# Optimization experiments

Hardware: AMD Instinct MI355X
Metric: run time of the kernel (lower is better)

## Reference

```python
import jax, jax.numpy as jnp
import numpy as np

N_USER = 200000
N_ITEM = 100000
E = 1000000
H = 128
IN_USER = 64
IN_ITEM = 128
OUT = 16
L = 2  # n_layers
NEG_SLOPE = 0.01  # F.leaky_relu default


def _leaky(x):
    return jnp.where(x >= 0, x, NEG_SLOPE * x)


def _sage(x_src, x_dst, src, dst, n_dst, Wl, bl, Wr):
    """PyG SAGEConv (aggr='mean'): lin_l(mean_{j->i} x_j) + lin_r(x_i)."""
    agg = jax.ops.segment_sum(x_src[src], dst, num_segments=n_dst)  # [n_dst, H]
    cnt = jax.ops.segment_sum(jnp.ones((src.shape[0],), x_src.dtype), dst, num_segments=n_dst)
    mean = agg / jnp.maximum(cnt, 1.0)[:, None]
    return mean @ Wl + bl + x_dst @ Wr


def setup_inputs() -> dict:
    key = jax.random.key(0)
    ks = jax.random.split(key, 32)
    s = 0.05
    inp = {
        "x_user": jax.random.normal(ks[0], (N_USER, IN_USER), jnp.float32),
        "x_item": jax.random.normal(ks[1], (N_ITEM, IN_ITEM), jnp.float32),
        "src_rates": jax.random.randint(ks[2], (E,), 0, N_USER, jnp.int32),
        "dst_rates": jax.random.randint(ks[3], (E,), 0, N_ITEM, jnp.int32),
        "src_rated": jax.random.randint(ks[4], (E,), 0, N_ITEM, jnp.int32),
        "dst_rated": jax.random.randint(ks[5], (E,), 0, N_USER, jnp.int32),
        "src_fol": jax.random.randint(ks[6], (E,), 0, N_USER, jnp.int32),
        "dst_fol": jax.random.randint(ks[7], (E,), 0, N_USER, jnp.int32),
        # input projections (per node type)
        "W_in_user": s * jax.random.normal(ks[8], (IN_USER, H), jnp.float32),
        "b_in_user": jnp.zeros((H,), jnp.float32),
        "W_in_item": s * jax.random.normal(ks[9], (IN_ITEM, H), jnp.float32),
        "b_in_item": jnp.zeros((H,), jnp.float32),
        # per-layer SAGEConv params, stacked over layers [L, ...]
        "Wl_rates": s * jax.random.normal(ks[10], (L, H, H), jnp.float32),
        "bl_rates": jnp.zeros((L, H), jnp.float32),
        "Wr_rates": s * jax.random.normal(ks[11], (L, H, H), jnp.float32),
        "Wl_rated": s * jax.random.normal(ks[12], (L, H, H), jnp.float32),
        "bl_rated": jnp.zeros((L, H), jnp.float32),
        "Wr_rated": s * jax.random.normal(ks[13], (L, H, H), jnp.float32),
        "Wl_fol": s * jax.random.normal(ks[14], (L, H, H), jnp.float32),
        "bl_fol": jnp.zeros((L, H), jnp.float32),
        "Wr_fol": s * jax.random.normal(ks[15], (L, H, H), jnp.float32),
        # output head
        "W_out": s * jax.random.normal(ks[16], (H, OUT), jnp.float32),
        "b_out": jnp.zeros((OUT,), jnp.float32),
    }
    return inp


def reference(x_user, x_item, src_rates, dst_rates, src_rated, dst_rated,
              src_fol, dst_fol, W_in_user, b_in_user, W_in_item, b_in_item,
              Wl_rates, bl_rates, Wr_rates, Wl_rated, bl_rated, Wr_rated,
              Wl_fol, bl_fol, Wr_fol, W_out, b_out):
    hu = x_user @ W_in_user + b_in_user  # [N_USER, H]
    hi = x_item @ W_in_item + b_in_item  # [N_ITEM, H]
    for l in range(L):
        # user->item ('rates')
        hi_new = _sage(hu, hi, src_rates, dst_rates, N_ITEM,
                       Wl_rates[l], bl_rates[l], Wr_rates[l])
        # item->user ('rated_by') + user->user ('follows'), HeteroConv aggr='sum'
        hu_new = (_sage(hi, hu, src_rated, dst_rated, N_USER,
                        Wl_rated[l], bl_rated[l], Wr_rated[l])
                  + _sage(hu, hu, src_fol, dst_fol, N_USER,
                          Wl_fol[l], bl_fol[l], Wr_fol[l]))
        hu, hi = hu_new, hi_new
        if l != L - 1:
            hu = _leaky(hu)
            hi = _leaky(hi)
    return hu @ W_out + b_out  # target_node == 'user'
```

## Files before the change

kernel.cpp:

```cpp
#include <hip/hip_runtime.h>
#include <cstdint>

typedef short short8 __attribute__((ext_vector_type(8)));
typedef float floatx4 __attribute__((ext_vector_type(4)));
typedef unsigned char uchar;

constexpr int NU = 200000;
constexpr int NI = 100000;
constexpr int NEDGE = 1000000;
constexpr int HD = 128;
constexpr int HH = HD * HD;
constexpr int BUK = 1024;
constexpr int EPB = 4096;
constexpr int EPT = 16;
constexpr int MAXBUK = 256;
constexpr int NBLK = (NEDGE + EPB - 1) / EPB;
constexpr int NB_I = (NI + BUK - 1) / BUK;
constexpr int NB_U = (NU + BUK - 1) / BUK;
constexpr int LROW = 136;

__device__ __forceinline__ float bits2f(short s) {
    return __uint_as_float(((unsigned int)(unsigned short)s) << 16);
}
__device__ __forceinline__ short f2bits(float f) {
    unsigned int u = __float_as_uint(f);
    unsigned int lsb = (u >> 16) & 1u;
    u += 0x7fffu + lsb;
    return (short)(u >> 16);
}

__global__ __launch_bounds__(256) void k_cnt3(const int* __restrict__ dst0,
                                              const int* __restrict__ dst1,
                                              const int* __restrict__ dst2,
                                              int* __restrict__ cnts) {
    __shared__ int cnt[MAXBUK];
    const int g = blockIdx.x / NBLK;
    const int blk = blockIdx.x % NBLK;
    const int* dst = (g == 0) ? dst0 : (g == 1) ? dst1 : dst2;
    int t = threadIdx.x;
    for (int b = t; b < MAXBUK; b += 256) cnt[b] = 0;
    __syncthreads();
    const int e0 = blk * EPB + t * EPT;
#pragma unroll
    for (int i = 0; i < EPT; ++i) {
        int e = e0 + i;
        if (e < NEDGE) atomicAdd(&cnt[dst[e] >> 10], 1);
    }
    __syncthreads();
    for (int b = t; b < MAXBUK; b += 256)
        cnts[(size_t)(g * NBLK + blk) * MAXBUK + b] = cnt[b];
}

__global__ __launch_bounds__(256) void k_bases3(const int* __restrict__ cnts,
                                                int* __restrict__ base,
                                                int* __restrict__ bbase,
                                                int* __restrict__ off0,
                                                int* __restrict__ off1,
                                                int* __restrict__ off2) {
    __shared__ int s[256];
    const int g = blockIdx.x;
    const int t = threadIdx.x;
    int tot = 0;
    for (int blk = 0; blk < NBLK; ++blk)
        tot += cnts[(size_t)(g * NBLK + blk) * MAXBUK + t];
    s[t] = tot;
    __syncthreads();
    for (int d = 1; d < 256; d <<= 1) {
        int u = (t >= d) ? s[t - d] : 0;
        __syncthreads();
        s[t] += u;
        __syncthreads();
    }
    int bb = s[t] - tot;
    bbase[g * 257 + t] = bb;
    if (t == 255) bbase[g * 257 + 256] = bb + tot;
    int run = bb;
    for (int blk = 0; blk < NBLK; ++blk) {
        size_t idx = (size_t)(g * NBLK + blk) * MAXBUK + t;
        base[idx] = run;
        run += cnts[idx];
    }
    if (t == 0) {
        if (g == 0) off0[NI] = NEDGE;
        else if (g == 1) off1[NU] = NEDGE;
        else off2[NU] = NEDGE;
    }
}

__global__ __launch_bounds__(256) void k_part3(const int* __restrict__ src0,
                                               const int* __restrict__ dst0,
                                               const int* __restrict__ src1,
                                               const int* __restrict__ dst1,
                                               const int* __restrict__ src2,
                                               const int* __restrict__ dst2,
                                               const int* __restrict__ base,
                                               int* __restrict__ pairs) {
    __shared__ int cnt[MAXBUK];
    __shared__ int bas[MAXBUK];
    const int g = blockIdx.x / NBLK;
    const int blk = blockIdx.x % NBLK;
    const int* src = (g == 0) ? src0 : (g == 1) ? src1 : src2;
    const int* dst = (g == 0) ? dst0 : (g == 1) ? dst1 : dst2;
    int* pg = pairs + (size_t)g * NEDGE;
    int t = threadIdx.x;
    for (int b = t; b < MAXBUK; b += 256) cnt[b] = 0;
    __syncthreads();
    const int e0 = blk * EPB + t * EPT;
    int sv[EPT], dv[EPT], rk[EPT];
#pragma unroll
    for (int i = 0; i < EPT; ++i) {
        int e = e0 + i;
        bool ok = e < NEDGE;
        dv[i] = ok ? dst[e] : 0;
        sv[i] = ok ? src[e] : 0;
    }
#pragma unroll
    for (int i = 0; i < EPT; ++i)
        rk[i] = (e0 + i < NEDGE) ? atomicAdd(&cnt[dv[i] >> 10], 1) : 0;
    __syncthreads();
    for (int b = t; b < MAXBUK; b += 256)
        bas[b] = base[(size_t)(g * NBLK + blk) * MAXBUK + b];
    __syncthreads();
#pragma unroll
    for (int i = 0; i < EPT; ++i) {
        if (e0 + i < NEDGE)
            pg[bas[dv[i] >> 10] + rk[i]] = sv[i] | ((dv[i] & 1023) << 18);
    }
}

__global__ __launch_bounds__(256) void k_place3(const int* __restrict__ pairs,
                                                const int* __restrict__ bbase,
                                                int* __restrict__ off0, int* __restrict__ esrc0,
                                                int* __restrict__ off1, int* __restrict__ esrc1,
                                                int* __restrict__ off2, int* __restrict__ esrc2) {
    __shared__ int cnt[BUK];
    __shared__ int ts[256];
    int bi = blockIdx.x;
    int g, bloc, N;
    int* off;
    int* esrc;
    if (bi < NB_I) { g = 0; bloc = bi; N = NI; off = off0; esrc = esrc0; }
    else if (bi < NB_I + NB_U) { g = 1; bloc = bi - NB_I; N = NU; off = off1; esrc = esrc1; }
    else { g = 2; bloc = bi - NB_I - NB_U; N = NU; off = off2; esrc = esrc2; }
    const int* pg = pairs + (size_t)g * NEDGE;
    const int b0 = bbase[g * 257 + bloc];
    const int b1 = bbase[g * 257 + bloc + 1];
    const int t = threadIdx.x;
    for (int i = t; i < BUK; i += 256) cnt[i] = 0;
    __syncthreads();
    for (int j = b0 + t; j < b1; j += 256) atomicAdd(&cnt[pg[j] >> 18], 1);
    __syncthreads();
    const int idx = t * 4;
    int c0 = cnt[idx], c1 = cnt[idx + 1], c2 = cnt[idx + 2], c3 = cnt[idx + 3];
    int ssum = c0 + c1 + c2 + c3;
    ts[t] = ssum;
    __syncthreads();
    for (int d = 1; d < 256; d <<= 1) {
        int u = (t >= d) ? ts[t - d] : 0;
        __syncthreads();
        ts[t] += u;
        __syncthreads();
    }
    int o = b0 + ts[t] - ssum;
    const int n0 = bloc * BUK;
    int cc[4] = {c0, c1, c2, c3};
#pragma unroll
    for (int i = 0; i < 4; ++i) {
        int n = n0 + idx + i;
        if (n < N) off[n] = o;
        cnt[idx + i] = o;
        o += cc[i];
    }
    __syncthreads();
    for (int j = b0 + t; j < b1; j += 256) {
        int p = pg[j];
        int pos = atomicAdd(&cnt[p >> 18], 1);
        esrc[pos] = p & 0x3FFFF;
    }
}

__global__ void k_pack(short* __restrict__ dst, const float* __restrict__ A,
                       const float* __restrict__ B, const float* __restrict__ B2,
                       int KA, int KBr, int NCOL) {
    int l = threadIdx.x;
    int kbt = (KA + KBr) >> 5;
    int nt = blockIdx.x / kbt;
    int kb = blockIdx.x % kbt;
    int col = nt * 16 + (l & 15);
    int k0 = kb * 32 + (l >> 4) * 8;
    short8 o;
#pragma unroll
    for (int j = 0; j < 8; ++j) {
        int k = k0 + j;
        float f;
        if (k < KA) {
            f = A[(size_t)k * NCOL + col];
        } else {
            int k2 = k - KA;
            f = B[(size_t)k2 * NCOL + col];
            if (B2) f += B2[(size_t)k2 * NCOL + col];
        }
        o[j] = f2bits(f);
    }
    *(short8*)(dst + ((size_t)blockIdx.x * 64 + l) * 8) = o;
}

__global__ void k_pack3(short* __restrict__ dst, const float* __restrict__ A,
                        const float* __restrict__ B, const float* __restrict__ C1,
                        const float* __restrict__ C2) {
    int l = threadIdx.x;
    constexpr int kbt = 12;
    int nt = blockIdx.x / kbt;
    int kb = blockIdx.x % kbt;
    int col = nt * 16 + (l & 15);
    int k0 = kb * 32 + (l >> 4) * 8;
    short8 o;
#pragma unroll
    for (int j = 0; j < 8; ++j) {
        int k = k0 + j;
        float f;
        if (k < 128) f = A[(size_t)k * 128 + col];
        else if (k < 256) f = B[(size_t)(k - 128) * 128 + col];
        else f = C1[(size_t)(k - 256) * 128 + col] + C2[(size_t)(k - 256) * 128 + col];
        o[j] = f2bits(f);
    }
    *(short8*)(dst + ((size_t)blockIdx.x * 64 + l) * 8) = o;
}

__global__ void k_foldW(float* __restrict__ dst, const float* __restrict__ Wa,
                        const float* __restrict__ Wb, const float* __restrict__ Wo,
                        int colOff, int NC) {
    int k = blockIdx.x;
    int c = threadIdx.x;
    float a = 0.f;
    for (int t = 0; t < 128; ++t) {
        float w = Wa[(size_t)k * 128 + t];
        if (Wb) w += Wb[(size_t)k * 128 + t];
        a += w * Wo[t * 16 + c];
    }
    dst[(size_t)k * NC + colOff + c] = a;
}

__global__ void k_bfold(float* __restrict__ dst, const float* __restrict__ bl1,
                        const float* __restrict__ bl2, const float* __restrict__ Wo,
                        const float* __restrict__ bo) {
    int c = threadIdx.x;
    float a = 0.f;
    for (int t = 0; t < 128; ++t) a += (bl1[t] + bl2[t]) * Wo[t * 16 + c];
    dst[c] = a + bo[c];
}

__global__ void k_addbias(float* __restrict__ dst, const float* __restrict__ a,
                          const float* __restrict__ b) {
    int i = threadIdx.x;
    dst[i] = a[i] + b[i];
}

__device__ __forceinline__ void gather_mean_u8(const uchar* __restrict__ X8,
                                               const float* __restrict__ scale,
                                               const int* __restrict__ off,
                                               const int* __restrict__ esrc,
                                               int ar, int g, float macc[4][8]) {
#pragma unroll
    for (int kb = 0; kb < 4; ++kb)
#pragma unroll
        for (int i = 0; i < 8; ++i) macc[kb][i] = 0.f;
    float S = 0.f;

    const int s = off[ar], e = off[ar + 1];
    for (int j = s; j < e; ++j) {
        const int i0 = esrc[j];
        const float s0 = scale[i0];
        const uchar* p0 = X8 + (size_t)i0 * HD + g * 8;
        S += s0;
#pragma unroll
        for (int kb = 0; kb < 4; ++kb) {
            uint2 v = *(const uint2*)(p0 + kb * 32);
#pragma unroll
            for (int i = 0; i < 4; ++i) {
                macc[kb][i]     = fmaf(s0, (float)((v.x >> (8 * i)) & 0xffu), macc[kb][i]);
                macc[kb][4 + i] = fmaf(s0, (float)((v.y >> (8 * i)) & 0xffu), macc[kb][4 + i]);
            }
        }
    }
    const int d = e - s;
    const float inv = 1.f / (float)(d > 0 ? d : 1);
    const float corr = 128.f * S;
#pragma unroll
    for (int kb = 0; kb < 4; ++kb)
#pragma unroll
        for (int i = 0; i < 8; ++i) macc[kb][i] = (macc[kb][i] - corr) * inv;
}

template <int NT2>
__device__ __forceinline__ void fold_epi(const floatx4* acc8, const float* __restrict__ bias,
                                         const short* __restrict__ pFold,
                                         short* __restrict__ Y, int r0, int lane,
                                         short* my, int M) {
    const int colL = lane & 15;
    const int g = lane >> 4;
#pragma unroll
    for (int nt = 0; nt < 8; ++nt) {
        float bv = bias[nt * 16 + colL];
#pragma unroll
        for (int r = 0; r < 4; ++r) {
            float x = acc8[nt][r] + bv;
            x = (x >= 0.f) ? x : 0.01f * x;
            my[(g * 4 + r) * LROW + nt * 16 + colL] = f2bits(x);
        }
    }
    short8 af[4];
    const short* rp = my + colL * LROW + g * 8;
#pragma unroll
    for (int kb = 0; kb < 4; ++kb) af[kb] = *(const short8*)(rp + kb * 32);

    floatx4 a2[NT2];
#pragma unroll
    for (int nt2 = 0; nt2 < NT2; ++nt2) a2[nt2] = (floatx4){0.f, 0.f, 0.f, 0.f};
    const short8* wp = (const short8*)pFold + lane;
#pragma unroll
    for (int nt2 = 0; nt2 < NT2; ++nt2)
#pragma unroll
        for (int kb = 0; kb < 4; ++kb) {
            short8 b = wp[(nt2 * 4 + kb) * 64];
            a2[nt2] = __builtin_amdgcn_mfma_f32_16x16x32_bf16(af[kb], b, a2[nt2], 0, 0, 0);
        }

    const int rbase = r0 + g * 4;
#pragma unroll
    for (int nt2 = 0; nt2 < NT2; ++nt2)
#pragma unroll
        for (int r = 0; r < 4; ++r) {
            int row = rbase + r;
            if (row < M) Y[(size_t)row * (NT2 * 16) + nt2 * 16 + colL] = f2bits(a2[nt2][r]);
        }
}

__global__ __launch_bounds__(256) void k_sage_all(
        const short* __restrict__ hu, const short* __restrict__ hi,
        const uchar* __restrict__ hu8, const float* __restrict__ scU,
        const uchar* __restrict__ hi8, const float* __restrict__ scI,
        const int* __restrict__ off_rates, const int* __restrict__ esrc_rates,
        const int* __restrict__ off_rated, const int* __restrict__ esrc_rated,
        const int* __restrict__ off_fol, const int* __restrict__ esrc_fol,
        const short* __restrict__ WpI, const float* __restrict__ biasI,
        const short* __restrict__ pYI,
        const short* __restrict__ WpU, const float* __restrict__ biasU,
        const short* __restrict__ pYU,
        short* __restrict__ YI, short* __restrict__ YZ, int gU) {
    __shared__ short stage[4 * 16 * LROW];
    const int lane = threadIdx.x & 63;
    const int wv = threadIdx.x >> 6;
    short* my = stage + wv * (16 * LROW);
    const int g = lane >> 4;
    const int ksub = g * 8;

    if ((int)blockIdx.x < gU) {
        const int r0 = blockIdx.x * 64 + wv * 16;
        int ar = r0 + (lane & 15);
        if (ar >= NU) ar = NU - 1;

        short8 afrag[12];
        {
            float macc[4][8];
            gather_mean_u8(hi8, scI, off_rated, esrc_rated, ar, g, macc);
#pragma unroll
            for (int kb = 0; kb < 4; ++kb) {
                short8 f;
#pragma unroll
                for (int i = 0; i < 8; ++i) f[i] = f2bits(macc[kb][i]);
                afrag[kb] = f;
            }
            gather_mean_u8(hu8, scU, off_fol, esrc_fol, ar, g, macc);
#pragma unroll
            for (int kb = 0; kb < 4; ++kb) {
                short8 f;
#pragma unroll
                for (int i = 0; i < 8; ++i) f[i] = f2bits(macc[kb][i]);
                afrag[4 + kb] = f;
            }
        }
        {
            const short* p = hu + (size_t)ar * HD + ksub;
#pragma unroll
            for (int kb = 0; kb < 4; ++kb) afrag[8 + kb] = *(const short8*)(p + kb * 32);
        }

        floatx4 acc[8];
#pragma unroll
        for (int nt = 0; nt < 8; ++nt) acc[nt] = (floatx4){0.f, 0.f, 0.f, 0.f};
        const short8* wp = (const short8*)WpU + lane;
#pragma unroll
        for (int nt = 0; nt < 8; ++nt)
#pragma unroll
            for (int kb = 0; kb < 12; ++kb) {
                short8 b = wp[(nt * 12 + kb) * 64];
                acc[nt] = __builtin_amdgcn_mfma_f32_16x16x32_bf16(afrag[kb], b, acc[nt], 0, 0, 0);
            }

        fold_epi<2>(acc, biasU, pYU, YZ, r0, lane, my, NU);
    } else {
        const int b = blockIdx.x - gU;
        const int r0 = b * 64 + wv * 16;
        int ar = r0 + (lane & 15);
        if (ar >= NI) ar = NI - 1;

        short8 afrag[8];
        {
            float macc[4][8];
            gather_mean_u8(hu8, scU, off_rates, esrc_rates, ar, g, macc);
#pragma unroll
            for (int kb = 0; kb < 4; ++kb) {
                short8 f;
#pragma unroll
                for (int i = 0; i < 8; ++i) f[i] = f2bits(macc[kb][i]);
                afrag[kb] = f;
            }
            const short* p = hi + (size_t)ar * HD + ksub;
#pragma unroll
            for (int kb = 0; kb < 4; ++kb) afrag[4 + kb] = *(const short8*)(p + kb * 32);
        }

        floatx4 acc[8];
#pragma unroll
        for (int nt = 0; nt < 8; ++nt) acc[nt] = (floatx4){0.f, 0.f, 0.f, 0.f};
        const short8* wp = (const short8*)WpI + lane;
#pragma unroll
        for (int nt = 0; nt < 8; ++nt)
#pragma unroll
            for (int kb = 0; kb < 8; ++kb) {
                short8 b = wp[(nt * 8 + kb) * 64];
                acc[nt] = __builtin_amdgcn_mfma_f32_16x16x32_bf16(afrag[kb], b, acc[nt], 0, 0, 0);
            }

        fold_epi<1>(acc, biasI, pYI, YI, r0, lane, my, NI);
    }
}

template <int KB1>
__device__ __forceinline__ void mm_body(int bid, const float* __restrict__ A1,
                                        const short* __restrict__ Wp,
                                        const float* __restrict__ bias,
                                        short* __restrict__ C,
                                        uchar* __restrict__ U8,
                                        float* __restrict__ scale, int M,
                                        int lane, int wv) {
    const int r0 = bid * 128 + wv * 32;
    const int g = lane >> 4;
    const int ksub = g * 8;
    const int colL = lane & 15;
    short8 afrag[2][KB1];
#pragma unroll
    for (int h = 0; h < 2; ++h) {
        int ar = r0 + h * 16 + colL;
        if (ar >= M) ar = M - 1;
        const float* p = A1 + (size_t)ar * (KB1 * 32) + ksub;
#pragma unroll
        for (int kb = 0; kb < KB1; ++kb) {
            short8 f;
#pragma unroll
            for (int j = 0; j < 8; ++j) f[j] = f2bits(p[kb * 32 + j]);
            afrag[h][kb] = f;
        }
    }
    floatx4 acc[2][8];
#pragma unroll
    for (int h = 0; h < 2; ++h)
#pragma unroll
        for (int nt = 0; nt < 8; ++nt) acc[h][nt] = (floatx4){0.f, 0.f, 0.f, 0.f};
    const short8* wp = (const short8*)Wp + lane;
#pragma unroll
    for (int nt = 0; nt < 8; ++nt)
#pragma unroll
        for (int kb = 0; kb < KB1; ++kb) {
            short8 b = wp[(nt * KB1 + kb) * 64];
            acc[0][nt] = __builtin_amdgcn_mfma_f32_16x16x32_bf16(afrag[0][kb], b, acc[0][nt], 0, 0, 0);
            acc[1][nt] = __builtin_amdgcn_mfma_f32_16x16x32_bf16(afrag[1][kb], b, acc[1][nt], 0, 0, 0);
        }
#pragma unroll
    for (int h = 0; h < 2; ++h) {
#pragma unroll
        for (int r = 0; r < 4; ++r) {
            const int row = r0 + h * 16 + g * 4 + r;
            float v[8];
            float m = 0.f;
#pragma unroll
            for (int nt = 0; nt < 8; ++nt) {
                v[nt] = acc[h][nt][r] + bias[nt * 16 + colL];
                m = fmaxf(m, fabsf(v[nt]));
            }
#pragma unroll
            for (int x = 1; x < 16; x <<= 1) m = fmaxf(m, __shfl_xor(m, x, 16));
            const float invq = (m > 0.f) ? 127.f / m : 0.f;
            if (row < M) {
#pragma unroll
                for (int nt = 0; nt < 8; ++nt) {
                    C[(size_t)row * HD + nt * 16 + colL] = f2bits(v[nt]);
                    U8[(size_t)row * HD + nt * 16 + colL] =
                        (uchar)((int)rintf(v[nt] * invq) + 128);
                }
                if (colL == 0) scale[row] = m * (1.f / 127.f);
            }
        }
    }
}

__global__ __launch_bounds__(256) void k_mm2(const float* __restrict__ xu,
                                             const short* __restrict__ pWu,
                                             const float* __restrict__ bu,
                                             short* __restrict__ hu,
                                             uchar* __restrict__ hu8,
                                             float* __restrict__ scU,
                                             const float* __restrict__ xi,
                                             const short* __restrict__ pWi,
                                             const float* __restrict__ bi,
                                             short* __restrict__ hi,
                                             uchar* __restrict__ hi8,
                                             float* __restrict__ scI, int gU2) {
    const int lane = threadIdx.x & 63;
    const int wv = threadIdx.x >> 6;
    if ((int)blockIdx.x < gU2)
        mm_body<2>(blockIdx.x, xu, pWu, bu, hu, hu8, scU, NU, lane, wv);
    else
        mm_body<4>(blockIdx.x - gU2, xi, pWi, bi, hi, hi8, scI, NI, lane, wv);
}

__global__ __launch_bounds__(256) void k_out(const short* __restrict__ YZ,
                                             const short* __restrict__ YI,
                                             const int* __restrict__ off_f,
                                             const int* __restrict__ esrc_f,
                                             const int* __restrict__ off_r,
                                             const int* __restrict__ esrc_r,
                                             const float* __restrict__ bias16,
                                             float* __restrict__ out, int N) {
    int t = threadIdx.x;
    int node = blockIdx.x * 128 + (t >> 1);
    int half = t & 1;
    if (node >= N) return;
    const int c0 = half * 8;

    float a[8] = {0.f, 0.f, 0.f, 0.f, 0.f, 0.f, 0.f, 0.f};
    {
        const int s = off_f[node], e = off_f[node + 1];
        int j = s;
        for (; j + 4 <= e; j += 4) {
            short8 v0 = *(const short8*)(YZ + (size_t)esrc_f[j] * 32 + c0);
            short8 v1 = *(const short8*)(YZ + (size_t)esrc_f[j + 1] * 32 + c0);
            short8 v2 = *(const short8*)(YZ + (size_t)esrc_f[j + 2] * 32 + c0);
            short8 v3 = *(const short8*)(YZ + (size_t)esrc_f[j + 3] * 32 + c0);
#pragma unroll
            for (int i = 0; i < 8; ++i)
                a[i] += (bits2f(v0[i]) + bits2f(v1[i])) + (bits2f(v2[i]) + bits2f(v3[i]));
        }
        for (; j < e; ++j) {
            short8 v = *(const short8*)(YZ + (size_t)esrc_f[j] * 32 + c0);
#pragma unroll
            for (int i = 0; i < 8; ++i) a[i] += bits2f(v[i]);
        }
        int d = e - s;
        float inv = 1.f / (float)(d > 0 ? d : 1);
#pragma unroll
        for (int i = 0; i < 8; ++i) a[i] *= inv;
    }
    {
        float b[8] = {0.f, 0.f, 0.f, 0.f, 0.f, 0.f, 0.f, 0.f};
        const int s = off_r[node], e = off_r[node + 1];
        int j = s;
        for (; j + 4 <= e; j += 4) {
            short8 v0 = *(const short8*)(YI + (size_t)esrc_r[j] * 16 + c0);
            short8 v1 = *(const short8*)(YI + (size_t)esrc_r[j + 1] * 16 + c0);
            short8 v2 = *(const short8*)(YI + (size_t)esrc_r[j + 2] * 16 + c0);
            short8 v3 = *(const short8*)(YI + (size_t)esrc_r[j + 3] * 16 + c0);
#pragma unroll
            for (int i = 0; i < 8; ++i)
                b[i] += (bits2f(v0[i]) + bits2f(v1[i])) + (bits2f(v2[i]) + bits2f(v3[i]));
        }
        for (; j < e; ++j) {
            short8 v = *(const short8*)(YI + (size_t)esrc_r[j] * 16 + c0);
#pragma unroll
            for (int i = 0; i < 8; ++i) b[i] += bits2f(v[i]);
        }
        int d = e - s;
        float inv = 1.f / (float)(d > 0 ? d : 1);
#pragma unroll
        for (int i = 0; i < 8; ++i) a[i] += b[i] * inv;
    }
    short8 z = *(const short8*)(YZ + (size_t)node * 32 + 16 + c0);
#pragma unroll
    for (int i = 0; i < 8; ++i)
        out[(size_t)node * 16 + c0 + i] = a[i] + bits2f(z[i]) + bias16[c0 + i];
}

extern "C" void kernel_launch(void* const* d_in, const int* in_sizes, int n_in,
                              void* d_out, int out_size, void* d_ws, size_t ws_size,
                              hipStream_t stream) {
    const float* x_user    = (const float*)d_in[0];
    const float* x_item    = (const float*)d_in[1];
    const int* src_rates   = (const int*)d_in[2];
    const int* dst_rates   = (const int*)d_in[3];
    const int* src_rated   = (const int*)d_in[4];
    const int* dst_rated   = (const int*)d_in[5];
    const int* src_fol     = (const int*)d_in[6];
    const int* dst_fol     = (const int*)d_in[7];
    const float* W_in_user = (const float*)d_in[8];
    const float* b_in_user = (const float*)d_in[9];
    const float* W_in_item = (const float*)d_in[10];
    const float* b_in_item = (const float*)d_in[11];
    const float* Wl_rates  = (const float*)d_in[12];
    const float* bl_rates  = (const float*)d_in[13];
    const float* Wr_rates  = (const float*)d_in[14];
    const float* Wl_rated  = (const float*)d_in[15];
    const float* bl_rated  = (const float*)d_in[16];
    const float* Wr_rated  = (const float*)d_in[17];
    const float* Wl_fol    = (const float*)d_in[18];
    const float* bl_fol    = (const float*)d_in[19];
    const float* Wr_fol    = (const float*)d_in[20];
    const float* W_out     = (const float*)d_in[21];
    const float* b_out     = (const float*)d_in[22];
    float* out = (float*)d_out;

    char* w = (char*)d_ws;
    size_t used = 0;
    auto alloc = [&](size_t bytes) -> void* {
        void* p = w + used;
        used += (bytes + 255) & ~(size_t)255;
        return p;
    };
    short* hu_a = (short*)alloc((size_t)NU * HD * 2);
    short* hi_a = (short*)alloc((size_t)NI * HD * 2);
    uchar* hu8  = (uchar*)alloc((size_t)NU * HD);
    uchar* hi8  = (uchar*)alloc((size_t)NI * HD);
    float* scU  = (float*)alloc((size_t)NU * 4);
    float* scI  = (float*)alloc((size_t)NI * 4);
    short* YZ   = (short*)alloc((size_t)NU * 32 * 2);
    short* YI   = (short*)alloc((size_t)NI * 16 * 2);

    int* off_rates  = (int*)alloc((size_t)(NI + 1) * 4);
    int* esrc_rates = (int*)alloc((size_t)NEDGE * 4);
    int* off_rated  = (int*)alloc((size_t)(NU + 1) * 4);
    int* esrc_rated = (int*)alloc((size_t)NEDGE * 4);
    int* off_fol    = (int*)alloc((size_t)(NU + 1) * 4);
    int* esrc_fol   = (int*)alloc((size_t)NEDGE * 4);
    int* pairs      = (int*)alloc((size_t)3 * NEDGE * 4);
    int* cnts       = (int*)alloc((size_t)3 * NBLK * MAXBUK * 4);
    int* base       = (int*)alloc((size_t)3 * NBLK * MAXBUK * 4);
    int* bbase      = (int*)alloc((size_t)3 * 257 * 4);

    short* pWu     = (short*)alloc(8 * 2 * 64 * 8 * 2);
    short* pWi     = (short*)alloc(8 * 4 * 64 * 8 * 2);
    short* pRates0 = (short*)alloc(8 * 8 * 64 * 8 * 2);
    short* pUser0  = (short*)alloc(8 * 12 * 64 * 8 * 2);
    float* WfU     = (float*)alloc(128 * 32 * 4);
    float* WfI     = (float*)alloc(128 * 16 * 4);
    short* pYU     = (short*)alloc(2 * 4 * 64 * 8 * 2);
    short* pYI     = (short*)alloc(1 * 4 * 64 * 8 * 2);
    float* bSum0   = (float*)alloc(128 * 4);
    float* bias16  = (float*)alloc(16 * 4);
    if (used > ws_size) return;

    k_cnt3<<<3 * NBLK, 256, 0, stream>>>(dst_rates, dst_rated, dst_fol, cnts);
    k_bases3<<<3, 256, 0, stream>>>(cnts, base, bbase, off_rates, off_rated, off_fol);
    k_part3<<<3 * NBLK, 256, 0, stream>>>(src_rates, dst_rates, src_rated, dst_rated,
                                          src_fol, dst_fol, base, pairs);
    k_place3<<<NB_I + 2 * NB_U, 256, 0, stream>>>(pairs, bbase,
                                                  off_rates, esrc_rates,
                                                  off_rated, esrc_rated,
                                                  off_fol, esrc_fol);

    k_pack<<<16, 64, 0, stream>>>(pWu, W_in_user, nullptr, nullptr, 64, 0, 128);
    k_pack<<<32, 64, 0, stream>>>(pWi, W_in_item, nullptr, nullptr, 128, 0, 128);
    k_pack<<<64, 64, 0, stream>>>(pRates0, Wl_rates, Wr_rates, nullptr, 128, 128, 128);
    k_pack3<<<96, 64, 0, stream>>>(pUser0, Wl_rated, Wl_fol, Wr_rated, Wr_fol);
    k_addbias<<<1, 128, 0, stream>>>(bSum0, bl_rated, bl_fol);
    k_foldW<<<128, 16, 0, stream>>>(WfU, Wl_fol + HH,   nullptr,     W_out, 0, 32);
    k_foldW<<<128, 16, 0, stream>>>(WfU, Wr_rated + HH, Wr_fol + HH, W_out, 16, 32);
    k_foldW<<<128, 16, 0, stream>>>(WfI, Wl_rated + HH, nullptr,     W_out, 0, 16);
    k_pack<<<8, 64, 0, stream>>>(pYU, WfU, nullptr, nullptr, 128, 0, 32);
    k_pack<<<4, 64, 0, stream>>>(pYI, WfI, nullptr, nullptr, 128, 0, 16);
    k_bfold<<<1, 16, 0, stream>>>(bias16, bl_rated + 128, bl_fol + 128, W_out, b_out);

    const int gU2 = (NU + 127) / 128;
    const int gI2 = (NI + 127) / 128;
    const int gU  = (NU + 63) / 64;
    const int gI  = (NI + 63) / 64;

    k_mm2<<<gU2 + gI2, 256, 0, stream>>>(x_user, pWu, b_in_user, hu_a, hu8, scU,
                                         x_item, pWi, b_in_item, hi_a, hi8, scI, gU2);

    k_sage_all<<<gU + gI, 256, 0, stream>>>(
        hu_a, hi_a, hu8, scU, hi8, scI,
        off_rates, esrc_rates, off_rated, esrc_rated, off_fol, esrc_fol,
        pRates0, bl_rates, pYI, pUser0, bSum0, pYU, YI, YZ, gU);

    k_out<<<(NU + 127) / 128, 256, 0, stream>>>(
        YZ, YI, off_fol, esrc_fol, off_rated, esrc_rated, bias16, out, NU);
}
```

Before: 494.8 us.

## Permute uint8 feature layout for 32-byte contiguous gathers and unroll edge loop by four

The quantized uint8 node features are now written in a permuted column order, so each lane group's 32 bytes are contiguous. The gather can then load two uint4 per neighbor instead of four strided uint2. The edge loop is also unrolled by four so several neighbor rows are loaded before the accumulate, which is meant to raise memory-level parallelism in the gather that dominates the runtime. This relies on the producer's permutation matching the consumer's macc index mapping, and the unroll costs extra registers.

Result: faster. 448.5 us (-9.4%).

```diff
diff --git a/kernel.cpp b/kernel.cpp
--- a/kernel.cpp
+++ b/kernel.cpp
@@ -256,6 +256,20 @@
     dst[i] = a[i] + b[i];
 }
 
+__device__ __forceinline__ void acc_u8(float macc[4][8], uint4 a, uint4 b, float s) {
+#pragma unroll
+    for (int i = 0; i < 4; ++i) {
+        macc[0][i]     = fmaf(s, (float)((a.x >> (8 * i)) & 0xffu), macc[0][i]);
+        macc[0][4 + i] = fmaf(s, (float)((a.y >> (8 * i)) & 0xffu), macc[0][4 + i]);
+        macc[1][i]     = fmaf(s, (float)((a.z >> (8 * i)) & 0xffu), macc[1][i]);
+        macc[1][4 + i] = fmaf(s, (float)((a.w >> (8 * i)) & 0xffu), macc[1][4 + i]);
+        macc[2][i]     = fmaf(s, (float)((b.x >> (8 * i)) & 0xffu), macc[2][i]);
+        macc[2][4 + i] = fmaf(s, (float)((b.y >> (8 * i)) & 0xffu), macc[2][4 + i]);
+        macc[3][i]     = fmaf(s, (float)((b.z >> (8 * i)) & 0xffu), macc[3][i]);
+        macc[3][4 + i] = fmaf(s, (float)((b.w >> (8 * i)) & 0xffu), macc[3][4 + i]);
+    }
+}
+
 __device__ __forceinline__ void gather_mean_u8(const uchar* __restrict__ X8,
                                                const float* __restrict__ scale,
                                                const int* __restrict__ off,
@@ -268,20 +282,31 @@
     float S = 0.f;
 
     const int s = off[ar], e = off[ar + 1];
-    for (int j = s; j < e; ++j) {
+    int j = s;
+    for (; j + 4 <= e; j += 4) {
+        const int i0 = esrc[j], i1 = esrc[j + 1], i2 = esrc[j + 2], i3 = esrc[j + 3];
+        const float s0 = scale[i0], s1 = scale[i1], s2 = scale[i2], s3 = scale[i3];
+        const uchar* p0 = X8 + (size_t)i0 * HD + g * 32;
+        const uchar* p1 = X8 + (size_t)i1 * HD + g * 32;
+        const uchar* p2 = X8 + (size_t)i2 * HD + g * 32;
+        const uchar* p3 = X8 + (size_t)i3 * HD + g * 32;
+        uint4 a0 = *(const uint4*)p0, b0 = *(const uint4*)(p0 + 16);
+        uint4 a1 = *(const uint4*)p1, b1 = *(const uint4*)(p1 + 16);
+        uint4 a2 = *(const uint4*)p2, b2 = *(const uint4*)(p2 + 16);
+        uint4 a3 = *(const uint4*)p3, b3 = *(const uint4*)(p3 + 16);
+        S += (s0 + s1) + (s2 + s3);
+        acc_u8(macc, a0, b0, s0);
+        acc_u8(macc, a1, b1, s1);
+        acc_u8(macc, a2, b2, s2);
+        acc_u8(macc, a3, b3, s3);
+    }
+    for (; j < e; ++j) {
         const int i0 = esrc[j];
         const float s0 = scale[i0];
-        const uchar* p0 = X8 + (size_t)i0 * HD + g * 8;
+        const uchar* p0 = X8 + (size_t)i0 * HD + g * 32;
+        uint4 a = *(const uint4*)p0, b = *(const uint4*)(p0 + 16);
         S += s0;
-#pragma unroll
-        for (int kb = 0; kb < 4; ++kb) {
-            uint2 v = *(const uint2*)(p0 + kb * 32);
-#pragma unroll
-            for (int i = 0; i < 4; ++i) {
-                macc[kb][i]     = fmaf(s0, (float)((v.x >> (8 * i)) & 0xffu), macc[kb][i]);
-                macc[kb][4 + i] = fmaf(s0, (float)((v.y >> (8 * i)) & 0xffu), macc[kb][4 + i]);
-            }
-        }
+        acc_u8(macc, a, b, s0);
     }
     const int d = e - s;
     const float inv = 1.f / (float)(d > 0 ? d : 1);
@@ -496,8 +521,9 @@
 #pragma unroll
                 for (int nt = 0; nt < 8; ++nt) {
                     C[(size_t)row * HD + nt * 16 + colL] = f2bits(v[nt]);
-                    U8[(size_t)row * HD + nt * 16 + colL] =
-                        (uchar)((int)rintf(v[nt] * invq) + 128);
+                    const int pp = (((nt & 1) * 2 + (colL >> 3)) << 5)
+                                 + ((nt >> 1) << 3) + (colL & 7);
+                    U8[(size_t)row * HD + pp] = (uchar)((int)rintf(v[nt] * invq) + 128);
                 }
                 if (colL == 0) scale[row] = m * (1.f / 127.f);
             }
```

## Restructure sage kernel: 16-lane-per-node gather, LDS tiles, split N across waves

Applied to the files above, without the earlier changes.

The fused SAGE kernel now assigns 16 lanes to each destination node, with each lane covering 8 channels, instead of one lane per node covering 32 channels. Each block handles 16 rows. The gathered means go through shared-memory tiles so the four waves can split the output column tiles of the MFMA GEMM between them. The gather loop is unrolled by four edges to raise memory-level parallelism, and the grid grows fourfold. This adds block-level syncs and leaves some waves idle during the small fold GEMM.

New measurement: 422.8 us, median of 2. 14.6% less time.

```diff
diff --git a/kernel.cpp b/kernel.cpp
--- a/kernel.cpp
+++ b/kernel.cpp
@@ -256,84 +256,52 @@
     dst[i] = a[i] + b[i];
 }
 
-__device__ __forceinline__ void gather_mean_u8(const uchar* __restrict__ X8,
-                                               const float* __restrict__ scale,
-                                               const int* __restrict__ off,
-                                               const int* __restrict__ esrc,
-                                               int ar, int g, float macc[4][8]) {
-#pragma unroll
-    for (int kb = 0; kb < 4; ++kb)
-#pragma unroll
-        for (int i = 0; i < 8; ++i) macc[kb][i] = 0.f;
+__device__ __forceinline__ void gmean8(const uchar* __restrict__ X8,
+                                       const float* __restrict__ scale,
+                                       const int* __restrict__ off,
+                                       const int* __restrict__ esrc,
+                                       int node, int ch, float m[8]) {
+#pragma unroll
+    for (int i = 0; i < 8; ++i) m[i] = 0.f;
     float S = 0.f;
-
-    const int s = off[ar], e = off[ar + 1];
-    for (int j = s; j < e; ++j) {
+    const int s = off[node], e = off[node + 1];
+    int j = s;
+    for (; j + 4 <= e; j += 4) {
+        const int i0 = esrc[j], i1 = esrc[j + 1], i2 = esrc[j + 2], i3 = esrc[j + 3];
+        const float s0 = scale[i0], s1 = scale[i1], s2 = scale[i2], s3 = scale[i3];
+        uint2 v0 = *(const uint2*)(X8 + (size_t)i0 * HD + ch * 8);
+        uint2 v1 = *(const uint2*)(X8 + (size_t)i1 * HD + ch * 8);
+        uint2 v2 = *(const uint2*)(X8 + (size_t)i2 * HD + ch * 8);
+        uint2 v3 = *(const uint2*)(X8 + (size_t)i3 * HD + ch * 8);
+        S += (s0 + s1) + (s2 + s3);
+#pragma unroll
+        for (int i = 0; i < 4; ++i) {
+            m[i]     += s0 * (float)((v0.x >> (8 * i)) & 0xffu)
+                      + s1 * (float)((v1.x >> (8 * i)) & 0xffu)
+                      + s2 * (float)((v2.x >> (8 * i)) & 0xffu)
+                      + s3 * (float)((v3.x >> (8 * i)) & 0xffu);
+            m[4 + i] += s0 * (float)((v0.y >> (8 * i)) & 0xffu)
+                      + s1 * (float)((v1.y >> (8 * i)) & 0xffu)
+                      + s2 * (float)((v2.y >> (8 * i)) & 0xffu)
+                      + s3 * (float)((v3.y >> (8 * i)) & 0xffu);
+        }
+    }
+    for (; j < e; ++j) {
         const int i0 = esrc[j];
         const float s0 = scale[i0];
-        const uchar* p0 = X8 + (size_t)i0 * HD + g * 8;
+        uint2 v = *(const uint2*)(X8 + (size_t)i0 * HD + ch * 8);
         S += s0;
 #pragma unroll
-        for (int kb = 0; kb < 4; ++kb) {
-            uint2 v = *(const uint2*)(p0 + kb * 32);
-#pragma unroll
-            for (int i = 0; i < 4; ++i) {
-                macc[kb][i]     = fmaf(s0, (float)((v.x >> (8 * i)) & 0xffu), macc[kb][i]);
-                macc[kb][4 + i] = fmaf(s0, (float)((v.y >> (8 * i)) & 0xffu), macc[kb][4 + i]);
-            }
+        for (int i = 0; i < 4; ++i) {
+            m[i]     = fmaf(s0, (float)((v.x >> (8 * i)) & 0xffu), m[i]);
+            m[4 + i] = fmaf(s0, (float)((v.y >> (8 * i)) & 0xffu), m[4 + i]);
         }
     }
     const int d = e - s;
     const float inv = 1.f / (float)(d > 0 ? d : 1);
     const float corr = 128.f * S;
 #pragma unroll
-    for (int kb = 0; kb < 4; ++kb)
-#pragma unroll
-        for (int i = 0; i < 8; ++i) macc[kb][i] = (macc[kb][i] - corr) * inv;
-}
-
-template <int NT2>
-__device__ __forceinline__ void fold_epi(const floatx4* acc8, const float* __restrict__ bias,
-                                         const short* __restrict__ pFold,
-                                         short* __restrict__ Y, int r0, int lane,
-                                         short* my, int M) {
-    const int colL = lane & 15;
-    const int g = lane >> 4;
-#pragma unroll
-    for (int nt = 0; nt < 8; ++nt) {
-        float bv = bias[nt * 16 + colL];
-#pragma unroll
-        for (int r = 0; r < 4; ++r) {
-            float x = acc8[nt][r] + bv;
-            x = (x >= 0.f) ? x : 0.01f * x;
-            my[(g * 4 + r) * LROW + nt * 16 + colL] = f2bits(x);
-        }
-    }
-    short8 af[4];
-    const short* rp = my + colL * LROW + g * 8;
-#pragma unroll
-    for (int kb = 0; kb < 4; ++kb) af[kb] = *(const short8*)(rp + kb * 32);
-
-    floatx4 a2[NT2];
-#pragma unroll
-    for (int nt2 = 0; nt2 < NT2; ++nt2) a2[nt2] = (floatx4){0.f, 0.f, 0.f, 0.f};
-    const short8* wp = (const short8*)pFold + lane;
-#pragma unroll
-    for (int nt2 = 0; nt2 < NT2; ++nt2)
-#pragma unroll
-        for (int kb = 0; kb < 4; ++kb) {
-            short8 b = wp[(nt2 * 4 + kb) * 64];
-            a2[nt2] = __builtin_amdgcn_mfma_f32_16x16x32_bf16(af[kb], b, a2[nt2], 0, 0, 0);
-        }
-
-    const int rbase = r0 + g * 4;
-#pragma unroll
-    for (int nt2 = 0; nt2 < NT2; ++nt2)
-#pragma unroll
-        for (int r = 0; r < 4; ++r) {
-            int row = rbase + r;
-            if (row < M) Y[(size_t)row * (NT2 * 16) + nt2 * 16 + colL] = f2bits(a2[nt2][r]);
-        }
+    for (int i = 0; i < 8; ++i) m[i] = (m[i] - corr) * inv;
 }
 
 __global__ __launch_bounds__(256) void k_sage_all(
@@ -348,92 +316,162 @@
         const short* __restrict__ WpU, const float* __restrict__ biasU,
         const short* __restrict__ pYU,
         short* __restrict__ YI, short* __restrict__ YZ, int gU) {
-    __shared__ short stage[4 * 16 * LROW];
+    __shared__ short tileA[16 * LROW];
+    __shared__ short tileB[16 * LROW];
+    __shared__ short tileO[16 * LROW];
     const int lane = threadIdx.x & 63;
     const int wv = threadIdx.x >> 6;
-    short* my = stage + wv * (16 * LROW);
+    const int nl = lane >> 4;
+    const int ch = lane & 15;
+    const int colL = lane & 15;
     const int g = lane >> 4;
-    const int ksub = g * 8;
 
     if ((int)blockIdx.x < gU) {
-        const int r0 = blockIdx.x * 64 + wv * 16;
-        int ar = r0 + (lane & 15);
-        if (ar >= NU) ar = NU - 1;
+        const int r0 = blockIdx.x * 16;
+        const int lnode = wv * 4 + nl;
+        int node = r0 + lnode;
+        if (node >= NU) node = NU - 1;
+
+        float m[8];
+        gmean8(hi8, scI, off_rated, esrc_rated, node, ch, m);
+#pragma unroll
+        for (int i = 0; i < 8; ++i) tileA[lnode * LROW + ch * 8 + i] = f2bits(m[i]);
+        gmean8(hu8, scU, off_fol, esrc_fol, node, ch, m);
+#pragma unroll
+        for (int i = 0; i < 8; ++i) tileB[lnode * LROW + ch * 8 + i] = f2bits(m[i]);
+        __syncthreads();
 
         short8 afrag[12];
         {
-            float macc[4][8];
-            gather_mean_u8(hi8, scI, off_rated, esrc_rated, ar, g, macc);
+            const short* ra = tileA + colL * LROW + g * 8;
+            const short* rb = tileB + colL * LROW + g * 8;
 #pragma unroll
             for (int kb = 0; kb < 4; ++kb) {
-                short8 f;
-#pragma unroll
-                for (int i = 0; i < 8; ++i) f[i] = f2bits(macc[kb][i]);
-                afrag[kb] = f;
-            }
-            gather_mean_u8(hu8, scU, off_fol, esrc_fol, ar, g, macc);
-#pragma unroll
-            for (int kb = 0; kb < 4; ++kb) {
-                short8 f;
-#pragma unroll
-                for (int i = 0; i < 8; ++i) f[i] = f2bits(macc[kb][i]);
-                afrag[4 + kb] = f;
-            }
-        }
-        {
-            const short* p = hu + (size_t)ar * HD + ksub;
+                afrag[kb] = *(const short8*)(ra + kb * 32);
+                afrag[4 + kb] = *(const short8*)(rb + kb * 32);
+            }
+            int ar = r0 + colL;
+            if (ar >= NU) ar = NU - 1;
+            const short* p = hu + (size_t)ar * HD + g * 8;
 #pragma unroll
             for (int kb = 0; kb < 4; ++kb) afrag[8 + kb] = *(const short8*)(p + kb * 32);
         }
 
-        floatx4 acc[8];
-#pragma unroll
-        for (int nt = 0; nt < 8; ++nt) acc[nt] = (floatx4){0.f, 0.f, 0.f, 0.f};
+        floatx4 acc[2];
+#pragma unroll
+        for (int t2 = 0; t2 < 2; ++t2) acc[t2] = (floatx4){0.f, 0.f, 0.f, 0.f};
         const short8* wp = (const short8*)WpU + lane;
 #pragma unroll
-        for (int nt = 0; nt < 8; ++nt)
+        for (int t2 = 0; t2 < 2; ++t2) {
+            const int nt = wv * 2 + t2;
 #pragma unroll
             for (int kb = 0; kb < 12; ++kb) {
                 short8 b = wp[(nt * 12 + kb) * 64];
-                acc[nt] = __builtin_amdgcn_mfma_f32_16x16x32_bf16(afrag[kb], b, acc[nt], 0, 0, 0);
-            }
-
-        fold_epi<2>(acc, biasU, pYU, YZ, r0, lane, my, NU);
+                acc[t2] = __builtin_amdgcn_mfma_f32_16x16x32_bf16(afrag[kb], b, acc[t2], 0, 0, 0);
+            }
+        }
+#pragma unroll
+        for (int t2 = 0; t2 < 2; ++t2) {
+            const int nt = wv * 2 + t2;
+            float bv = biasU[nt * 16 + colL];
+#pragma unroll
+            for (int r = 0; r < 4; ++r) {
+                float x = acc[t2][r] + bv;
+                x = (x >= 0.f) ? x : 0.01f * x;
+                tileO[(g * 4 + r) * LROW + nt * 16 + colL] = f2bits(x);
+            }
+        }
+        __syncthreads();
+
+        if (wv < 2) {
+            short8 af[4];
+            const short* rp = tileO + colL * LROW + g * 8;
+#pragma unroll
+            for (int kb = 0; kb < 4; ++kb) af[kb] = *(const short8*)(rp + kb * 32);
+            floatx4 a2 = (floatx4){0.f, 0.f, 0.f, 0.f};
+            const short8* fp = (const short8*)pYU + lane;
+#pragma unroll
+            for (int kb = 0; kb < 4; ++kb) {
+                short8 b = fp[(wv * 4 + kb) * 64];
+                a2 = __builtin_amdgcn_mfma_f32_16x16x32_bf16(af[kb], b, a2, 0, 0, 0);
+            }
+            const int rbase = r0 + g * 4;
+#pragma unroll
+            for (int r = 0; r < 4; ++r) {
+                int row = rbase + r;
+                if (row < NU) YZ[(size_t)row * 32 + wv * 16 + colL] = f2bits(a2[r]);
+            }
+        }
     } else {
         const int b = blockIdx.x - gU;
-        const int r0 = b * 64 + wv * 16;
-        int ar = r0 + (lane & 15);
-        if (ar >= NI) ar = NI - 1;
+        const int r0 = b * 16;
+        const int lnode = wv * 4 + nl;
+        int node = r0 + lnode;
+        if (node >= NI) node = NI - 1;
+
+        float m[8];
+        gmean8(hu8, scU, off_rates, esrc_rates, node, ch, m);
+#pragma unroll
+        for (int i = 0; i < 8; ++i) tileA[lnode * LROW + ch * 8 + i] = f2bits(m[i]);
+        __syncthreads();
 
         short8 afrag[8];
         {
-            float macc[4][8];
-            gather_mean_u8(hu8, scU, off_rates, esrc_rates, ar, g, macc);
-#pragma unroll
-            for (int kb = 0; kb < 4; ++kb) {
-                short8 f;
-#pragma unroll
-                for (int i = 0; i < 8; ++i) f[i] = f2bits(macc[kb][i]);
-                afrag[kb] = f;
-            }
-            const short* p = hi + (size_t)ar * HD + ksub;
+            const short* ra = tileA + colL * LROW + g * 8;
+#pragma unroll
+            for (int kb = 0; kb < 4; ++kb) afrag[kb] = *(const short8*)(ra + kb * 32);
+            int ar = r0 + colL;
+            if (ar >= NI) ar = NI - 1;
+            const short* p = hi + (size_t)ar * HD + g * 8;
 #pragma unroll
             for (int kb = 0; kb < 4; ++kb) afrag[4 + kb] = *(const short8*)(p + kb * 32);
         }
 
-        floatx4 acc[8];
-#pragma unroll
-        for (int nt = 0; nt < 8; ++nt) acc[nt] = (floatx4){0.f, 0.f, 0.f, 0.f};
+        floatx4 acc[2];
+#pragma unroll
+        for (int t2 = 0; t2 < 2; ++t2) acc[t2] = (floatx4){0.f, 0.f, 0.f, 0.f};
         const short8* wp = (const short8*)WpI + lane;
 #pragma unroll
-        for (int nt = 0; nt < 8; ++nt)
+        for (int t2 = 0; t2 < 2; ++t2) {
+            const int nt = wv * 2 + t2;
 #pragma unroll
             for (int kb = 0; kb < 8; ++kb) {
                 short8 b = wp[(nt * 8 + kb) * 64];
-                acc[nt] = __builtin_amdgcn_mfma_f32_16x16x32_bf16(afrag[kb], b, acc[nt], 0, 0, 0);
-            }
-
-        fold_epi<1>(acc, biasI, pYI, YI, r0, lane, my, NI);
+                acc[t2] = __builtin_amdgcn_mfma_f32_16x16x32_bf16(afrag[kb], b, acc[t2], 0, 0, 0);
+            }
+        }
+#pragma unroll
+        for (int t2 = 0; t2 < 2; ++t2) {
+            const int nt = wv * 2 + t2;
+            float bv = biasI[nt * 16 + colL];
+#pragma unroll
+            for (int r = 0; r < 4; ++r) {
+                float x = acc[t2][r] + bv;
+                x = (x >= 0.f) ? x : 0.01f * x;
+                tileO[(g * 4 + r) * LROW + nt * 16 + colL] = f2bits(x);
+            }
+        }
+        __syncthreads();
+
+        if (wv == 0) {
+            short8 af[4];
+            const short* rp = tileO + colL * LROW + g * 8;
+#pragma unroll
+            for (int kb = 0; kb < 4; ++kb) af[kb] = *(const short8*)(rp + kb * 32);
+            floatx4 a2 = (floatx4){0.f, 0.f, 0.f, 0.f};
+            const short8* fp = (const short8*)pYI + lane;
+#pragma unroll
+            for (int kb = 0; kb < 4; ++kb) {
+                short8 b = fp[kb * 64];
+                a2 = __builtin_amdgcn_mfma_f32_16x16x32_bf16(af[kb], b, a2, 0, 0, 0);
+            }
+            const int rbase = r0 + g * 4;
+#pragma unroll
+            for (int r = 0; r < 4; ++r) {
+                int row = rbase + r;
+                if (row < NI) YI[(size_t)row * 16 + colL] = f2bits(a2[r]);
+            }
+        }
     }
 }
 
@@ -681,8 +719,8 @@
 
     const int gU2 = (NU + 127) / 128;
     const int gI2 = (NI + 127) / 128;
-    const int gU  = (NU + 63) / 64;
-    const int gI  = (NI + 63) / 64;
+    const int gU  = (NU + 15) / 16;
+    const int gI  = (NI + 15) / 16;
 
     k_mm2<<<gU2 + gI2, 256, 0, stream>>>(x_user, pWu, b_in_user, hu_a, hu8, scU,
                                          x_item, pWi, b_in_item, hi_a, hi8, scI, gU2);
```
